# Kernel optimization log

Hardware: AMD Instinct MI355X
Metric: run time of the kernel (lower is better)

The kernel has to match this reference:

```python
import jax, jax.numpy as jnp
import numpy as np

N_FEAT = 350; D = 512; L = 4; DS = 64; NREG = 6; REG_E = 32
B = 32; S = 2048
CLAMP = 20.0


def _ln(x, g, b, eps=1e-5):
    mu = jnp.mean(x, axis=-1, keepdims=True)
    var = jnp.mean(jnp.square(x - mu), axis=-1, keepdims=True)
    return (x - mu) * jax.lax.rsqrt(var + eps) * g + b


def _slstm(x, ln_g, ln_b, Wi, bi, Wf, bf, Wz, bz, Wo, bo, Wp, bp):
    # x: [B,S,D] -> out: [B,S,D]
    xn = _ln(x, ln_g, ln_b)
    log_i = jnp.clip(jnp.einsum('bsd,de->bse', xn, Wi) + bi, -CLAMP, CLAMP)
    log_f = jnp.clip(jnp.einsum('bsd,de->bse', xn, Wf) + bf, -CLAMP, CLAMP)
    z = jnp.tanh(jnp.einsum('bsd,de->bse', xn, Wz) + bz)
    o = jax.nn.sigmoid(jnp.einsum('bsd,de->bse', xn, Wo) + bo)

    def step(carry, inp):
        m, c = carry
        li, lf, zt, ot = inp
        m_new = jnp.maximum(m + lf, li)
        i_s = jnp.exp(li - m_new)
        f_s = jnp.exp(m + lf - m_new)
        c_new = f_s * c + i_s * zt
        h = ot * jnp.tanh(c_new)
        return (m_new, c_new), h

    bsz = x.shape[0]
    init = (jnp.zeros((bsz, DS), x.dtype), jnp.zeros((bsz, DS), x.dtype))
    seq = (jnp.swapaxes(log_i, 0, 1), jnp.swapaxes(log_f, 0, 1),
           jnp.swapaxes(z, 0, 1), jnp.swapaxes(o, 0, 1))
    _, hs = jax.lax.scan(step, init, seq)  # hs: [S,B,DS]
    hs = jnp.swapaxes(hs, 0, 1)  # [B,S,DS]
    return jnp.einsum('bse,ed->bsd', hs, Wp) + bp


def setup_inputs() -> dict:
    key = jax.random.key(0)
    ks = iter(jax.random.split(key, 64))
    def p(*shape):
        return jax.random.normal(next(ks), shape, dtype=jnp.float32) * 0.02
    return {
        'x': jax.random.normal(next(ks), (B, S, N_FEAT), dtype=jnp.float32),
        'regime_ids': jax.random.randint(next(ks), (B, S), 0, NREG),
        'emb_regime': p(NREG, REG_E),
        'grn_w1': p(N_FEAT + REG_E, D), 'grn_b1': jnp.zeros((D,), jnp.float32),
        'grn_w2': p(D, N_FEAT), 'grn_b2': jnp.zeros((N_FEAT,), jnp.float32),
        'in_w': p(N_FEAT, D), 'in_b': jnp.zeros((D,), jnp.float32),
        'ln_in_g': jnp.ones((L, D), jnp.float32), 'ln_in_b': jnp.zeros((L, D), jnp.float32),
        'wi': p(L, D, DS), 'bi': jnp.zeros((L, DS), jnp.float32),
        'wf': p(L, D, DS), 'bf': jnp.zeros((L, DS), jnp.float32),
        'wz': p(L, D, DS), 'bz': jnp.zeros((L, DS), jnp.float32),
        'wo': p(L, D, DS), 'bo': jnp.zeros((L, DS), jnp.float32),
        'wp': p(L, DS, D), 'bp': jnp.zeros((L, D), jnp.float32),
        'nm_g': jnp.ones((L, D), jnp.float32), 'nm_b': jnp.zeros((L, D), jnp.float32),
        'hd15_w': p(D, 1), 'hd15_b': jnp.zeros((1,), jnp.float32),
        'hd30_w': p(D, 1), 'hd30_b': jnp.zeros((1,), jnp.float32),
        'hv_w': p(D, 3), 'hv_b': jnp.zeros((3,), jnp.float32),
        'hreg_w': p(D, NREG), 'hreg_b': jnp.zeros((NREG,), jnp.float32),
        'hrng_w': p(D, 3), 'hrng_b': jnp.zeros((3,), jnp.float32),
    }


def reference(x, regime_ids, emb_regime, grn_w1, grn_b1, grn_w2, grn_b2,
              in_w, in_b, ln_in_g, ln_in_b, wi, bi, wf, bf, wz, bz, wo, bo,
              wp, bp, nm_g, nm_b, hd15_w, hd15_b, hd30_w, hd30_b,
              hv_w, hv_b, hreg_w, hreg_b, hrng_w, hrng_b):
    # Variable selection network (regime-conditioned feature weights)
    remb = emb_regime[regime_ids]                      # [B,S,32]
    comb = jnp.concatenate([x, remb], axis=-1)         # [B,S,382]
    hidden = jax.nn.elu(jnp.einsum('bsf,fd->bsd', comb, grn_w1) + grn_b1)
    weights = jax.nn.softmax(jnp.einsum('bsd,df->bsf', hidden, grn_w2) + grn_b2, axis=-1)
    xw = x * weights
    h = jnp.einsum('bsf,fd->bsd', xw, in_w) + in_b     # [B,S,D]
    for l in range(L):
        res = _slstm(h, ln_in_g[l], ln_in_b[l], wi[l], bi[l], wf[l], bf[l],
                     wz[l], bz[l], wo[l], bo[l], wp[l], bp[l])
        h = _ln(h + res, nm_g[l], nm_b[l])
    h_last = h[:, -1, :]
    return (jnp.squeeze(h_last @ hd15_w + hd15_b, -1),
            jnp.squeeze(h_last @ hd30_w + hd30_b, -1),
            h_last @ hv_w + hv_b,
            h_last @ hreg_w + hreg_b,
            h_last @ hrng_w + hrng_b,
            h_last,
            weights[:, -1, :])
```

## Files before the change

### kernel.cpp

```cpp
#include <hip/hip_runtime.h>
#include <cmath>

#define NFEAT 350
#define DMODEL 512
#define NLAYER 4
#define DSZ 64
#define REG_E 32
#define BATCH 32
#define SEQ 2048
#define MTOK (BATCH * SEQ)
#define CLAMP_V 20.0f

#define CHUNK 64
#define NCHUNK (SEQ / CHUNK)

typedef short bf16x8 __attribute__((ext_vector_type(8)));
typedef float f32x4 __attribute__((ext_vector_type(4)));

__device__ __forceinline__ unsigned short f2b(float v) {
    union { float f; unsigned int u; } x; x.f = v;
    unsigned int r = x.u + 0x7fffu + ((x.u >> 16) & 1u);
    return (unsigned short)(r >> 16);
}
__device__ __forceinline__ float b2f(unsigned short u) {
    union { unsigned int i; float f; } x; x.i = ((unsigned int)u) << 16;
    return x.f;
}
__device__ __forceinline__ unsigned int pack2(float a, float b) {
    return ((unsigned int)f2b(b) << 16) | f2b(a);
}

__global__ __launch_bounds__(256) void tconv_k(const float* __restrict__ src,
                                               unsigned short* __restrict__ dst,
                                               int K, int N, int Kpad) {
    int k = blockIdx.x * 256 + threadIdx.x;
    int n = blockIdx.y;
    if (k >= Kpad) return;
    float v = (k < K && n < N) ? src[(size_t)k * N + n] : 0.f;
    dst[(size_t)n * Kpad + k] = f2b(v);
}

__global__ __launch_bounds__(256) void tconv_g_k(const float* __restrict__ wi,
                                                 const float* __restrict__ wf,
                                                 const float* __restrict__ wz,
                                                 const float* __restrict__ wo,
                                                 unsigned short* __restrict__ dstH,
                                                 unsigned short* __restrict__ dstL) {
    int k = blockIdx.x * 256 + threadIdx.x;
    int n = blockIdx.y;
    int z = blockIdx.z;
    int l = z >> 2, g = z & 3;
    const float* src = (g == 0 ? wi : g == 1 ? wf : g == 2 ? wz : wo) + (size_t)l * DMODEL * DSZ;
    float v = src[(size_t)k * DSZ + n];
    unsigned short hi = f2b(v);
    unsigned short lo = f2b(v - b2f(hi));
    dstH[(size_t)z * 32768 + (size_t)n * 512 + k] = hi;
    dstL[(size_t)z * 32768 + (size_t)n * 512 + k] = lo;
}

__global__ __launch_bounds__(1024) void gbias_k(const float* bi, const float* bf_,
                                                const float* bz, const float* bo,
                                                float* __restrict__ gbias) {
    int t = threadIdx.x;
    int l = t >> 8, r = t & 255, g = r >> 6, e = r & 63;
    const float* s = (g == 0 ? bi : g == 1 ? bf_ : g == 2 ? bz : bo);
    gbias[t] = s[l * 64 + e];
}

__global__ __launch_bounds__(256) void build_xc_k(const float* __restrict__ x,
                                                  const int* __restrict__ rid,
                                                  const float* __restrict__ emb,
                                                  unsigned short* __restrict__ xc) {
    int i = blockIdx.x * 256 + threadIdx.x;
    int m = i / 192, p = i - m * 192;
    int k = p * 2;
    float a = 0.f, b = 0.f;
    if (k < 350) {
        const float2 v = *(const float2*)(x + (size_t)m * NFEAT + k);
        a = v.x; b = v.y;
    } else if (k < 382) {
        int r = rid[m];
        const float2 v = *(const float2*)(emb + r * REG_E + (k - 350));
        a = v.x; b = v.y;
    }
    ((unsigned int*)xc)[(size_t)m * 192 + p] = pack2(a, b);
}

template <int ALD, int EPI>
__global__ __launch_bounds__(256) void mgemm_k(const unsigned short* __restrict__ Ab,
                                               const float* __restrict__ Af,
                                               const unsigned short* __restrict__ Bt,
                                               const float* __restrict__ bias,
                                               float* __restrict__ Cf,
                                               unsigned short* __restrict__ Cb,
                                               const float* __restrict__ muA,
                                               const float* __restrict__ rstdA,
                                               const float* __restrict__ lng,
                                               const float* __restrict__ lnb,
                                               int lda, int ldb, int K, int N, int ldc) {
    __shared__ unsigned short As[128][40];
    __shared__ unsigned short Bs[128][40];
    const int tid = threadIdx.x;
    const int lane = tid & 63;
    const int wave = tid >> 6;
    const int l15 = lane & 15;
    const int quad = lane >> 4;
    const int wm = (wave >> 1) * 64;
    const int wn = (wave & 1) * 64;
    const size_t m0 = (size_t)blockIdx.y * 128;
    const int n0 = blockIdx.x * 128;

    const int sr = tid >> 2;
    const int ku = tid & 3;

    const unsigned short* Br0 = Bt + ((size_t)(n0 + sr)) * ldb + ku * 8;
    const unsigned short* Br1 = Br0 + (size_t)64 * ldb;
    const unsigned short* Ar0 = Ab + (m0 + sr) * (size_t)lda + ku * 8;
    const unsigned short* Ar1 = Ar0 + (size_t)64 * lda;

    f32x4 acc[4][4] = {};

    for (int k0 = 0; k0 < K; k0 += 32) {
        *(uint4*)&As[sr][ku * 8]      = *(const uint4*)(Ar0 + k0);
        *(uint4*)&As[sr + 64][ku * 8] = *(const uint4*)(Ar1 + k0);
        *(uint4*)&Bs[sr][ku * 8]      = *(const uint4*)(Br0 + k0);
        *(uint4*)&Bs[sr + 64][ku * 8] = *(const uint4*)(Br1 + k0);
        __syncthreads();
        bf16x8 af[4], bf[4];
#pragma unroll
        for (int mt = 0; mt < 4; mt++)
            af[mt] = *(const bf16x8*)&As[wm + mt * 16 + l15][quad * 8];
#pragma unroll
        for (int nt = 0; nt < 4; nt++)
            bf[nt] = *(const bf16x8*)&Bs[wn + nt * 16 + l15][quad * 8];
#pragma unroll
        for (int mt = 0; mt < 4; mt++)
#pragma unroll
            for (int nt = 0; nt < 4; nt++)
                acc[mt][nt] = __builtin_amdgcn_mfma_f32_16x16x32_bf16(af[mt], bf[nt], acc[mt][nt], 0, 0, 0);
        __syncthreads();
    }

#pragma unroll
    for (int mt = 0; mt < 4; mt++) {
        int gmb = wm + mt * 16 + quad * 4;
#pragma unroll
        for (int nt = 0; nt < 4; nt++) {
            int gn = n0 + wn + nt * 16 + l15;
            if (gn < N) {
                float bv = bias[gn];
#pragma unroll
                for (int r = 0; r < 4; r++) {
                    size_t gm = m0 + gmb + r;
                    float v = acc[mt][nt][r] + bv;
                    if (EPI == 0) {
                        v = v > 0.f ? v : expm1f(v);
                        Cb[gm * (size_t)ldc + gn] = f2b(v);
                    } else if (EPI == 1) {
                        Cb[gm * (size_t)ldc + gn] = f2b(v);
                    } else {
                        Cf[gm * (size_t)ldc + gn] = v;
                    }
                }
            }
        }
    }
}

__global__ __launch_bounds__(256) void ggemm_k(const float* __restrict__ h,
                                               const unsigned short* __restrict__ BtH,
                                               const unsigned short* __restrict__ BtL,
                                               const float* __restrict__ bias,
                                               const float* __restrict__ mu,
                                               const float* __restrict__ rstd,
                                               const float* __restrict__ lng,
                                               const float* __restrict__ lnb,
                                               float* __restrict__ gates) {
    __shared__ unsigned short AsH[64][40];
    __shared__ unsigned short AsL[64][40];
    __shared__ unsigned short BsH[128][40];
    __shared__ unsigned short BsL[128][40];
    const int tid = threadIdx.x;
    const int lane = tid & 63;
    const int wave = tid >> 6;
    const int l15 = lane & 15;
    const int quad = lane >> 4;
    const int wm = (wave >> 1) * 32;
    const int wn = (wave & 1) * 64;
    const size_t m0 = (size_t)blockIdx.y * 64;
    const int n0 = blockIdx.x * 128;

    const int sr = tid >> 2;
    const int ku = tid & 3;
    const float* Ar = h + (m0 + sr) * (size_t)DMODEL + ku * 8;
    const float muv = mu[m0 + sr];
    const float rsv = rstd[m0 + sr];

    const int br = tid >> 1;
    const int kh = (tid & 1) * 16;
    const unsigned short* BH = BtH + (size_t)(n0 + br) * 512 + kh;
    const unsigned short* BL = BtL + (size_t)(n0 + br) * 512 + kh;

    float4 a0 = *(const float4*)(Ar);
    float4 a1 = *(const float4*)(Ar + 4);
    uint4 vh0 = *(const uint4*)(BH);
    uint4 vh1 = *(const uint4*)(BH + 8);
    uint4 vl0 = *(const uint4*)(BL);
    uint4 vl1 = *(const uint4*)(BL + 8);

    f32x4 acc[2][4] = {};

    for (int k0 = 0; k0 < DMODEL; k0 += 32) {
        {
            float4 g0 = *(const float4*)(lng + k0 + ku * 8);
            float4 g1 = *(const float4*)(lng + k0 + ku * 8 + 4);
            float4 c0 = *(const float4*)(lnb + k0 + ku * 8);
            float4 c1 = *(const float4*)(lnb + k0 + ku * 8 + 4);
            float v[8];
            v[0] = (a0.x - muv) * rsv * g0.x + c0.x;
            v[1] = (a0.y - muv) * rsv * g0.y + c0.y;
            v[2] = (a0.z - muv) * rsv * g0.z + c0.z;
            v[3] = (a0.w - muv) * rsv * g0.w + c0.w;
            v[4] = (a1.x - muv) * rsv * g1.x + c1.x;
            v[5] = (a1.y - muv) * rsv * g1.y + c1.y;
            v[6] = (a1.z - muv) * rsv * g1.z + c1.z;
            v[7] = (a1.w - muv) * rsv * g1.w + c1.w;
            unsigned int hw[4], lw[4];
#pragma unroll
            for (int j = 0; j < 4; j++) {
                unsigned short h0 = f2b(v[2 * j]);
                unsigned short h1 = f2b(v[2 * j + 1]);
                unsigned short l0 = f2b(v[2 * j] - b2f(h0));
                unsigned short l1 = f2b(v[2 * j + 1] - b2f(h1));
                hw[j] = (unsigned int)h0 | ((unsigned int)h1 << 16);
                lw[j] = (unsigned int)l0 | ((unsigned int)l1 << 16);
            }
            *(uint4*)&AsH[sr][ku * 8] = *(uint4*)hw;
            *(uint4*)&AsL[sr][ku * 8] = *(uint4*)lw;
        }
        *(uint4*)&BsH[br][kh]     = vh0;
        *(uint4*)&BsH[br][kh + 8] = vh1;
        *(uint4*)&BsL[br][kh]     = vl0;
        *(uint4*)&BsL[br][kh + 8] = vl1;
        __syncthreads();

        if (k0 + 32 < DMODEL) {
            a0 = *(const float4*)(Ar + k0 + 32);
            a1 = *(const float4*)(Ar + k0 + 36);
            vh0 = *(const uint4*)(BH + k0 + 32);
            vh1 = *(const uint4*)(BH + k0 + 40);
            vl0 = *(const uint4*)(BL + k0 + 32);
            vl1 = *(const uint4*)(BL + k0 + 40);
        }

        bf16x8 ah[2], al[2], bh[4], bl[4];
#pragma unroll
        for (int mt = 0; mt < 2; mt++) {
            ah[mt] = *(const bf16x8*)&AsH[wm + mt * 16 + l15][quad * 8];
            al[mt] = *(const bf16x8*)&AsL[wm + mt * 16 + l15][quad * 8];
        }
#pragma unroll
        for (int nt = 0; nt < 4; nt++) {
            bh[nt] = *(const bf16x8*)&BsH[wn + nt * 16 + l15][quad * 8];
            bl[nt] = *(const bf16x8*)&BsL[wn + nt * 16 + l15][quad * 8];
        }
#pragma unroll
        for (int mt = 0; mt < 2; mt++)
#pragma unroll
            for (int nt = 0; nt < 4; nt++) {
                acc[mt][nt] = __builtin_amdgcn_mfma_f32_16x16x32_bf16(ah[mt], bh[nt], acc[mt][nt], 0, 0, 0);
                acc[mt][nt] = __builtin_amdgcn_mfma_f32_16x16x32_bf16(al[mt], bh[nt], acc[mt][nt], 0, 0, 0);
                acc[mt][nt] = __builtin_amdgcn_mfma_f32_16x16x32_bf16(ah[mt], bl[nt], acc[mt][nt], 0, 0, 0);
            }
        __syncthreads();
    }

#pragma unroll
    for (int mt = 0; mt < 2; mt++) {
        int gmb = wm + mt * 16 + quad * 4;
#pragma unroll
        for (int nt = 0; nt < 4; nt++) {
            int gn = n0 + wn + nt * 16 + l15;
            float bv = bias[gn];
            int g = gn >> 6;
#pragma unroll
            for (int r = 0; r < 4; r++) {
                size_t gm = m0 + gmb + r;
                float v = acc[mt][nt][r] + bv;
                if (g < 2) v = fminf(fmaxf(v, -CLAMP_V), CLAMP_V);
                else if (g == 2) v = tanhf(v);
                else v = 1.f / (1.f + expf(-v));
                gates[gm * 256 + gn] = v;
            }
        }
    }
}

__global__ __launch_bounds__(256) void softmax_xw_k(const unsigned short* __restrict__ logits,
                                                    unsigned short* __restrict__ xc,
                                                    float* __restrict__ out_wlast) {
    int tok = blockIdx.x * 4 + (threadIdx.x >> 6);
    int lane = threadIdx.x & 63;
    const unsigned short* lr = logits + (size_t)tok * NFEAT;
    unsigned short* xr = xc + (size_t)tok * 384;
    float v[6];
    float mx = -1e30f;
#pragma unroll
    for (int i = 0; i < 6; i++) {
        int idx = lane + 64 * i;
        v[i] = (idx < NFEAT) ? b2f(lr[idx]) : -1e30f;
        mx = fmaxf(mx, v[i]);
    }
#pragma unroll
    for (int o = 32; o > 0; o >>= 1) mx = fmaxf(mx, __shfl_xor(mx, o, 64));
    float s = 0.f;
#pragma unroll
    for (int i = 0; i < 6; i++) { v[i] = expf(v[i] - mx); s += v[i]; }
#pragma unroll
    for (int o = 32; o > 0; o >>= 1) s += __shfl_xor(s, o, 64);
    float inv = 1.f / s;
    bool last = ((tok & (SEQ - 1)) == SEQ - 1);
    int b = tok >> 11;
#pragma unroll
    for (int i = 0; i < 6; i++) {
        int idx = lane + 64 * i;
        if (idx < NFEAT) {
            float w = v[i] * inv;
            xr[idx] = f2b(w * b2f(xr[idx]));
            if (last) out_wlast[b * NFEAT + idx] = w;
        } else if (idx < 352) {
            xr[idx] = 0;
        }
    }
}

__global__ __launch_bounds__(256) void ln_stats_k(const float* __restrict__ h,
                                                  float* __restrict__ mu,
                                                  float* __restrict__ rstd) {
    int tok = blockIdx.x * 4 + (threadIdx.x >> 6);
    int lane = threadIdx.x & 63;
    const float* row = h + (size_t)tok * DMODEL;
    float s = 0.f, sq = 0.f;
#pragma unroll
    for (int i = 0; i < 8; i++) {
        float v = row[lane + 64 * i];
        s += v;
        sq += v * v;
    }
#pragma unroll
    for (int o = 32; o > 0; o >>= 1) {
        s += __shfl_xor(s, o, 64);
        sq += __shfl_xor(sq, o, 64);
    }
    if (lane == 0) {
        float m = s * (1.f / DMODEL);
        float var = sq * (1.f / DMODEL) - m * m;
        mu[tok] = m;
        rstd[tok] = rsqrtf(var + 1e-5f);
    }
}

__global__ __launch_bounds__(256) void seg_agg_k(const float* __restrict__ gates,
                                                 float* __restrict__ aggF,
                                                 float* __restrict__ aggL,
                                                 float* __restrict__ aggS) {
    int b = blockIdx.x >> 3;
    int cg = blockIdx.x & 7;
    int chunk = cg * 4 + (threadIdx.x >> 6);
    int e = threadIdx.x & 63;
    const float* gp = gates + ((size_t)b * SEQ + (size_t)chunk * CHUNK) * 256;
    float F = 0.f, L = -1e30f, s = 0.f;
#pragma unroll 4
    for (int t = 0; t < CHUNK; t++) {
        const float* q = gp + (size_t)t * 256;
        float li = q[e], lf = q[64 + e], z = q[128 + e];
        float Ln = fmaxf(L + lf, li);
        s = expf(L + lf - Ln) * s + expf(li - Ln) * z;
        L = Ln;
        F += lf;
    }
    int idx = (b * NCHUNK + chunk) * 64 + e;
    aggF[idx] = F; aggL[idx] = L; aggS[idx] = s;
}

__global__ __launch_bounds__(64) void chunk_scan_k(const float* __restrict__ aggF,
                                                   const float* __restrict__ aggL,
                                                   const float* __restrict__ aggS,
                                                   float* __restrict__ stM,
                                                   float* __restrict__ stC) {
    int b = blockIdx.x;
    int e = threadIdx.x;
    float m = 0.f, c = 0.f;
    for (int k = 0; k < NCHUNK; k++) {
        int idx = (b * NCHUNK + k) * 64 + e;
        stM[idx] = m; stC[idx] = c;
        float F = aggF[idx], L = aggL[idx], s = aggS[idx];
        float mn = fmaxf(m + F, L);
        c = expf(m + F - mn) * c + expf(L - mn) * s;
        m = mn;
    }
}

__global__ __launch_bounds__(256) void replay_k(const float* __restrict__ gates,
                                                const float* __restrict__ stM,
                                                const float* __restrict__ stC,
                                                float* __restrict__ hs) {
    int b = blockIdx.x >> 3;
    int cg = blockIdx.x & 7;
    int chunk = cg * 4 + (threadIdx.x >> 6);
    int e = threadIdx.x & 63;
    int s0 = chunk * CHUNK;
    const float* gp = gates + ((size_t)b * SEQ + s0) * 256;
    float* hp = hs + ((size_t)b * SEQ + s0) * DSZ;
    int idx = (b * NCHUNK + chunk) * 64 + e;
    float m = stM[idx], c = stC[idx];
#pragma unroll 4
    for (int t = 0; t < CHUNK; t++) {
        const float* q = gp + (size_t)t * 256;
        float li = q[e], lf = q[64 + e], z = q[128 + e], o = q[192 + e];
        float mlf = m + lf;
        float mn = fmaxf(mlf, li);
        c = expf(mlf - mn) * c + expf(li - mn) * z;
        m = mn;
        hp[(size_t)t * DSZ + e] = o * tanhf(c);
    }
}

__global__ __launch_bounds__(256) void outproj_k(const float* __restrict__ hs,
                                                 const float* __restrict__ wp,
                                                 const float* __restrict__ bp,
                                                 const float* __restrict__ nmg,
                                                 const float* __restrict__ nmb,
                                                 float* __restrict__ h,
                                                 float* __restrict__ mu,
                                                 float* __restrict__ rstd) {
    __shared__ float shs[16][DSZ];
    __shared__ float swp[16][DMODEL];
    int wv = threadIdx.x >> 6;
    int lane = threadIdx.x & 63;
    int tok0 = blockIdx.x * 16;

    {
        const float4* src = (const float4*)(hs + (size_t)tok0 * DSZ);
        ((float4*)&shs[0][0])[threadIdx.x] = src[threadIdx.x];
    }
    __syncthreads();

    float acc[4][8] = {};
    for (int k0 = 0; k0 < DSZ; k0 += 16) {
        const float4* src = (const float4*)(wp + (size_t)k0 * DMODEL);
#pragma unroll
        for (int i = 0; i < 8; i++)
            ((float4*)&swp[0][0])[threadIdx.x + i * 256] = src[threadIdx.x + i * 256];
        __syncthreads();
#pragma unroll
        for (int k = 0; k < 16; k++) {
            float bv[8];
#pragma unroll
            for (int j = 0; j < 8; j++) bv[j] = swp[k][lane + 64 * j];
#pragma unroll
            for (int t = 0; t < 4; t++) {
                float av = shs[wv * 4 + t][k0 + k];
#pragma unroll
                for (int j = 0; j < 8; j++) acc[t][j] += av * bv[j];
            }
        }
        __syncthreads();
    }

#pragma unroll
    for (int t = 0; t < 4; t++) {
        int tok = tok0 + wv * 4 + t;
        float u[8];
        float s = 0.f, sq = 0.f;
#pragma unroll
        for (int j = 0; j < 8; j++) {
            int col = lane + 64 * j;
            float v = h[(size_t)tok * DMODEL + col] + acc[t][j] + bp[col];
            u[j] = v;
            s += v; sq += v * v;
        }
#pragma unroll
        for (int o = 32; o > 0; o >>= 1) { s += __shfl_xor(s, o, 64); sq += __shfl_xor(sq, o, 64); }
        float mean = s * (1.f / DMODEL);
        float var = sq * (1.f / DMODEL) - mean * mean;
        float rs = rsqrtf(var + 1e-5f);
        float s2 = 0.f, sq2 = 0.f;
#pragma unroll
        for (int j = 0; j < 8; j++) {
            int col = lane + 64 * j;
            float v = (u[j] - mean) * rs * nmg[col] + nmb[col];
            h[(size_t)tok * DMODEL + col] = v;
            s2 += v; sq2 += v * v;
        }
#pragma unroll
        for (int o = 32; o > 0; o >>= 1) { s2 += __shfl_xor(s2, o, 64); sq2 += __shfl_xor(sq2, o, 64); }
        if (lane == 0) {
            float m2 = s2 * (1.f / DMODEL);
            float v2 = sq2 * (1.f / DMODEL) - m2 * m2;
            mu[tok] = m2;
            rstd[tok] = rsqrtf(v2 + 1e-5f);
        }
    }
}

__global__ __launch_bounds__(64) void heads_k(const float* __restrict__ h,
                                              const float* hd15_w, const float* hd15_b,
                                              const float* hd30_w, const float* hd30_b,
                                              const float* hv_w, const float* hv_b,
                                              const float* hreg_w, const float* hreg_b,
                                              const float* hrng_w, const float* hrng_b,
                                              float* __restrict__ out) {
    int b = blockIdx.x;
    int lane = threadIdx.x;
    __shared__ float row[DMODEL];
    const float* hp = h + (size_t)(b * SEQ + SEQ - 1) * DMODEL;
#pragma unroll
    for (int i = 0; i < 8; i++) row[lane + 64 * i] = hp[lane + 64 * i];
    __syncthreads();
#pragma unroll
    for (int i = 0; i < 8; i++) out[448 + b * DMODEL + lane + 64 * i] = row[lane + 64 * i];
    if (lane < 14) {
        const float* w; const float* bb;
        int ncol, j, off;
        if (lane == 0)      { w = hd15_w; bb = hd15_b; ncol = 1; j = 0;         off = 0 + b; }
        else if (lane == 1) { w = hd30_w; bb = hd30_b; ncol = 1; j = 0;         off = 32 + b; }
        else if (lane < 5)  { j = lane - 2;  w = hv_w;   bb = hv_b;   ncol = 3; off = 64 + b * 3 + j; }
        else if (lane < 11) { j = lane - 5;  w = hreg_w; bb = hreg_b; ncol = 6; off = 160 + b * 6 + j; }
        else                { j = lane - 11; w = hrng_w; bb = hrng_b; ncol = 3; off = 352 + b * 3 + j; }
        float s = bb[j];
        for (int k = 0; k < DMODEL; k++) s += row[k] * w[k * ncol + j];
        out[off] = s;
    }
}

extern "C" void kernel_launch(void* const* d_in, const int* in_sizes, int n_in,
                              void* d_out, int out_size, void* d_ws, size_t ws_size,
                              hipStream_t stream) {
    (void)in_sizes; (void)n_in; (void)out_size; (void)ws_size;
    const float* x      = (const float*)d_in[0];
    const int*   rid    = (const int*)d_in[1];
    const float* emb    = (const float*)d_in[2];
    const float* grn_w1 = (const float*)d_in[3];
    const float* grn_b1 = (const float*)d_in[4];
    const float* grn_w2 = (const float*)d_in[5];
    const float* grn_b2 = (const float*)d_in[6];
    const float* in_w   = (const float*)d_in[7];
    const float* in_b   = (const float*)d_in[8];
    const float* ln_g   = (const float*)d_in[9];
    const float* ln_b   = (const float*)d_in[10];
    const float* wi     = (const float*)d_in[11];
    const float* bi     = (const float*)d_in[12];
    const float* wf     = (const float*)d_in[13];
    const float* bf_    = (const float*)d_in[14];
    const float* wz     = (const float*)d_in[15];
    const float* bz     = (const float*)d_in[16];
    const float* wo     = (const float*)d_in[17];
    const float* bo     = (const float*)d_in[18];
    const float* wp     = (const float*)d_in[19];
    const float* bp     = (const float*)d_in[20];
    const float* nm_g   = (const float*)d_in[21];
    const float* nm_b   = (const float*)d_in[22];

    float* out = (float*)d_out;
    char* W = (char*)d_ws;

    float* h               = (float*)W;
    unsigned short* hidden = (unsigned short*)W;
    unsigned short* logits = (unsigned short*)(W + 67108864);
    char* RB = W + 134217728;
    unsigned short* xc = (unsigned short*)RB;
    float* gates  = (float*)RB;
    float* hsbuf  = (float*)(RB + 67108864);
    char* RM = W + 218103808;
    float* aggF  = (float*)(RM);
    float* aggL  = (float*)(RM + 262144);
    float* aggS  = (float*)(RM + 524288);
    float* stM   = (float*)(RM + 786432);
    float* stC   = (float*)(RM + 1048576);
    float* mu    = (float*)(RM + 1310720);
    float* rstd  = (float*)(RM + 1572864);
    unsigned short* w1t  = (unsigned short*)(RM + 1835008);
    unsigned short* w2t  = (unsigned short*)(RM + 2228224);
    unsigned short* inwt = (unsigned short*)(RM + 2621440);
    unsigned short* gwtH = (unsigned short*)(RM + 2981888);
    unsigned short* gwtL = (unsigned short*)(RM + 4030464);
    float* gbias         = (float*)(RM + 5079040);

    build_xc_k<<<MTOK * 192 / 256, 256, 0, stream>>>(x, rid, emb, xc);
    tconv_k<<<dim3(2, 512), 256, 0, stream>>>(grn_w1, w1t, 382, 512, 384);
    tconv_k<<<dim3(2, 384), 256, 0, stream>>>(grn_w2, w2t, 512, 350, 512);
    tconv_k<<<dim3(2, 512), 256, 0, stream>>>(in_w, inwt, 350, 512, 352);
    tconv_g_k<<<dim3(2, 64, 16), 256, 0, stream>>>(wi, wf, wz, wo, gwtH, gwtL);
    gbias_k<<<1, 1024, 0, stream>>>(bi, bf_, bz, bo, gbias);

    mgemm_k<0, 0><<<dim3(4, 512), 256, 0, stream>>>(xc, nullptr, w1t, grn_b1, nullptr, hidden,
                                                    nullptr, nullptr, nullptr, nullptr,
                                                    384, 384, 384, 512, 512);
    mgemm_k<0, 1><<<dim3(3, 512), 256, 0, stream>>>(hidden, nullptr, w2t, grn_b2, nullptr, logits,
                                                    nullptr, nullptr, nullptr, nullptr,
                                                    512, 512, 512, 350, 350);
    softmax_xw_k<<<MTOK / 4, 256, 0, stream>>>(logits, xc, out + 16832);
    mgemm_k<0, 3><<<dim3(4, 512), 256, 0, stream>>>(xc, nullptr, inwt, in_b, h, nullptr,
                                                    nullptr, nullptr, nullptr, nullptr,
                                                    384, 352, 352, 512, 512);
    ln_stats_k<<<MTOK / 4, 256, 0, stream>>>(h, mu, rstd);

    for (int l = 0; l < NLAYER; l++) {
        ggemm_k<<<dim3(2, 1024), 256, 0, stream>>>(h,
                                                   gwtH + (size_t)l * 131072,
                                                   gwtL + (size_t)l * 131072,
                                                   gbias + l * 256,
                                                   mu, rstd,
                                                   ln_g + l * DMODEL, ln_b + l * DMODEL,
                                                   gates);
        seg_agg_k<<<BATCH * 8, 256, 0, stream>>>(gates, aggF, aggL, aggS);
        chunk_scan_k<<<BATCH, 64, 0, stream>>>(aggF, aggL, aggS, stM, stC);
        replay_k<<<BATCH * 8, 256, 0, stream>>>(gates, stM, stC, hsbuf);

        outproj_k<<<MTOK / 16, 256, 0, stream>>>(hsbuf,
                                                 wp + (size_t)l * DSZ * DMODEL,
                                                 bp + l * DMODEL,
                                                 nm_g + l * DMODEL,
                                                 nm_b + l * DMODEL,
                                                 h, mu, rstd);
    }

    heads_k<<<BATCH, 64, 0, stream>>>(h,
                                      (const float*)d_in[23], (const float*)d_in[24],
                                      (const float*)d_in[25], (const float*)d_in[26],
                                      (const float*)d_in[27], (const float*)d_in[28],
                                      (const float*)d_in[29], (const float*)d_in[30],
                                      (const float*)d_in[31], (const float*)d_in[32],
                                      out);
}
```

Measured before the change: 1.483 ms.

## Fuse chunk aggregation into gate GEMM with full-width N tiles

The gate GEMM now computes all 256 gate columns per 64-token block, so each block owns one full chunk. The per-chunk scan aggregate (F, L, s) is then computed in the epilogue from a shared-memory copy of the gates, and the separate seg_agg kernel, which re-read the gates from global memory, is removed. The cost is that each block now loads the whole weight tile, carries larger accumulators and uses about 52KB of shared memory. That lowers occupancy and halves the grid size. The unused mgemm_k template parameter and its arguments are also dropped.

Result: slower. 1.900 ms (+28.1%).

```diff
diff --git a/kernel.cpp b/kernel.cpp
--- a/kernel.cpp
+++ b/kernel.cpp
@@ -86,17 +86,12 @@
     ((unsigned int*)xc)[(size_t)m * 192 + p] = pack2(a, b);
 }
 
-template <int ALD, int EPI>
+template <int EPI>
 __global__ __launch_bounds__(256) void mgemm_k(const unsigned short* __restrict__ Ab,
-                                               const float* __restrict__ Af,
                                                const unsigned short* __restrict__ Bt,
                                                const float* __restrict__ bias,
                                                float* __restrict__ Cf,
                                                unsigned short* __restrict__ Cb,
-                                               const float* __restrict__ muA,
-                                               const float* __restrict__ rstdA,
-                                               const float* __restrict__ lng,
-                                               const float* __restrict__ lnb,
                                                int lda, int ldb, int K, int N, int ldc) {
     __shared__ unsigned short As[128][40];
     __shared__ unsigned short Bs[128][40];
@@ -175,20 +170,24 @@
                                                const float* __restrict__ rstd,
                                                const float* __restrict__ lng,
                                                const float* __restrict__ lnb,
-                                               float* __restrict__ gates) {
-    __shared__ unsigned short AsH[64][40];
-    __shared__ unsigned short AsL[64][40];
-    __shared__ unsigned short BsH[128][40];
-    __shared__ unsigned short BsL[128][40];
+                                               float* __restrict__ gates,
+                                               float* __restrict__ aggF,
+                                               float* __restrict__ aggL,
+                                               float* __restrict__ aggS) {
+    __shared__ __align__(16) char smem[53248];
+    unsigned short* AsH = (unsigned short*)smem;
+    unsigned short* AsL = AsH + 2560;
+    unsigned short* BsH = (unsigned short*)(smem + 10240);
+    unsigned short* BsL = BsH + 10240;
+    float* CP = (float*)smem;
+    float* SG = (float*)(smem + 49152);
+
     const int tid = threadIdx.x;
     const int lane = tid & 63;
     const int wave = tid >> 6;
     const int l15 = lane & 15;
     const int quad = lane >> 4;
-    const int wm = (wave >> 1) * 32;
-    const int wn = (wave & 1) * 64;
-    const size_t m0 = (size_t)blockIdx.y * 64;
-    const int n0 = blockIdx.x * 128;
+    const size_t m0 = (size_t)blockIdx.x * 64;
 
     const int sr = tid >> 2;
     const int ku = tid & 3;
@@ -196,19 +195,19 @@
     const float muv = mu[m0 + sr];
     const float rsv = rstd[m0 + sr];
 
-    const int br = tid >> 1;
-    const int kh = (tid & 1) * 16;
-    const unsigned short* BH = BtH + (size_t)(n0 + br) * 512 + kh;
-    const unsigned short* BL = BtL + (size_t)(n0 + br) * 512 + kh;
+    const unsigned short* BH = BtH + (size_t)tid * 512;
+    const unsigned short* BL = BtL + (size_t)tid * 512;
 
     float4 a0 = *(const float4*)(Ar);
     float4 a1 = *(const float4*)(Ar + 4);
-    uint4 vh0 = *(const uint4*)(BH);
-    uint4 vh1 = *(const uint4*)(BH + 8);
-    uint4 vl0 = *(const uint4*)(BL);
-    uint4 vl1 = *(const uint4*)(BL + 8);
-
-    f32x4 acc[2][4] = {};
+    uint4 vh[4], vl[4];
+#pragma unroll
+    for (int j = 0; j < 4; j++) {
+        vh[j] = *(const uint4*)(BH + j * 8);
+        vl[j] = *(const uint4*)(BL + j * 8);
+    }
+
+    f32x4 acc[4][4] = {};
 
     for (int k0 = 0; k0 < DMODEL; k0 += 32) {
         {
@@ -235,37 +234,40 @@
                 hw[j] = (unsigned int)h0 | ((unsigned int)h1 << 16);
                 lw[j] = (unsigned int)l0 | ((unsigned int)l1 << 16);
             }
-            *(uint4*)&AsH[sr][ku * 8] = *(uint4*)hw;
-            *(uint4*)&AsL[sr][ku * 8] = *(uint4*)lw;
-        }
-        *(uint4*)&BsH[br][kh]     = vh0;
-        *(uint4*)&BsH[br][kh + 8] = vh1;
-        *(uint4*)&BsL[br][kh]     = vl0;
-        *(uint4*)&BsL[br][kh + 8] = vl1;
+            *(uint4*)&AsH[sr * 40 + ku * 8] = *(uint4*)hw;
+            *(uint4*)&AsL[sr * 40 + ku * 8] = *(uint4*)lw;
+        }
+#pragma unroll
+        for (int j = 0; j < 4; j++) {
+            *(uint4*)&BsH[tid * 40 + j * 8] = vh[j];
+            *(uint4*)&BsL[tid * 40 + j * 8] = vl[j];
+        }
         __syncthreads();
 
         if (k0 + 32 < DMODEL) {
             a0 = *(const float4*)(Ar + k0 + 32);
             a1 = *(const float4*)(Ar + k0 + 36);
-            vh0 = *(const uint4*)(BH + k0 + 32);
-            vh1 = *(const uint4*)(BH + k0 + 40);
-            vl0 = *(const uint4*)(BL + k0 + 32);
-            vl1 = *(const uint4*)(BL + k0 + 40);
-        }
-
-        bf16x8 ah[2], al[2], bh[4], bl[4];
-#pragma unroll
-        for (int mt = 0; mt < 2; mt++) {
-            ah[mt] = *(const bf16x8*)&AsH[wm + mt * 16 + l15][quad * 8];
-            al[mt] = *(const bf16x8*)&AsL[wm + mt * 16 + l15][quad * 8];
+#pragma unroll
+            for (int j = 0; j < 4; j++) {
+                vh[j] = *(const uint4*)(BH + k0 + 32 + j * 8);
+                vl[j] = *(const uint4*)(BL + k0 + 32 + j * 8);
+            }
+        }
+
+        bf16x8 ah[4], al[4], bh[4], bl[4];
+#pragma unroll
+        for (int mt = 0; mt < 4; mt++) {
+            ah[mt] = *(const bf16x8*)&AsH[(mt * 16 + l15) * 40 + quad * 8];
+            al[mt] = *(const bf16x8*)&AsL[(mt * 16 + l15) * 40 + quad * 8];
         }
 #pragma unroll
         for (int nt = 0; nt < 4; nt++) {
-            bh[nt] = *(const bf16x8*)&BsH[wn + nt * 16 + l15][quad * 8];
-            bl[nt] = *(const bf16x8*)&BsL[wn + nt * 16 + l15][quad * 8];
-        }
-#pragma unroll
-        for (int mt = 0; mt < 2; mt++)
+            int brow = wave * 64 + nt * 16 + l15;
+            bh[nt] = *(const bf16x8*)&BsH[brow * 40 + quad * 8];
+            bl[nt] = *(const bf16x8*)&BsL[brow * 40 + quad * 8];
+        }
+#pragma unroll
+        for (int mt = 0; mt < 4; mt++)
 #pragma unroll
             for (int nt = 0; nt < 4; nt++) {
                 acc[mt][nt] = __builtin_amdgcn_mfma_f32_16x16x32_bf16(ah[mt], bh[nt], acc[mt][nt], 0, 0, 0);
@@ -276,23 +278,60 @@
     }
 
 #pragma unroll
-    for (int mt = 0; mt < 2; mt++) {
-        int gmb = wm + mt * 16 + quad * 4;
+    for (int mt = 0; mt < 4; mt++) {
 #pragma unroll
         for (int nt = 0; nt < 4; nt++) {
-            int gn = n0 + wn + nt * 16 + l15;
-            float bv = bias[gn];
-            int g = gn >> 6;
+            int e = nt * 16 + l15;
+            int col = wave * 64 + e;
+            float bv = bias[col];
 #pragma unroll
             for (int r = 0; r < 4; r++) {
-                size_t gm = m0 + gmb + r;
+                int row = mt * 16 + quad * 4 + r;
                 float v = acc[mt][nt][r] + bv;
-                if (g < 2) v = fminf(fmaxf(v, -CLAMP_V), CLAMP_V);
-                else if (g == 2) v = tanhf(v);
+                if (wave < 2) v = fminf(fmaxf(v, -CLAMP_V), CLAMP_V);
+                else if (wave == 2) v = tanhf(v);
                 else v = 1.f / (1.f + expf(-v));
-                gates[gm * 256 + gn] = v;
+                gates[(m0 + row) * 256 + col] = v;
+                if (wave < 3) CP[wave * 4096 + row * 64 + e] = v;
             }
         }
+    }
+    __syncthreads();
+
+    {
+        int e = tid & 63;
+        int seg = tid >> 6;
+        float F = 0.f, L = -1e30f, s = 0.f;
+#pragma unroll 4
+        for (int j = 0; j < 16; j++) {
+            int tt = seg * 16 + j;
+            float li = CP[tt * 64 + e];
+            float lf = CP[4096 + tt * 64 + e];
+            float z  = CP[8192 + tt * 64 + e];
+            float Ln = fmaxf(L + lf, li);
+            s = expf(L + lf - Ln) * s + expf(li - Ln) * z;
+            L = Ln;
+            F += lf;
+        }
+        SG[seg * 64 + e]       = F;
+        SG[256 + seg * 64 + e] = L;
+        SG[512 + seg * 64 + e] = s;
+    }
+    __syncthreads();
+    if (tid < 64) {
+        float F = 0.f, L = -1e30f, s = 0.f;
+#pragma unroll
+        for (int k = 0; k < 4; k++) {
+            float Fk = SG[k * 64 + tid];
+            float Lk = SG[256 + k * 64 + tid];
+            float sk = SG[512 + k * 64 + tid];
+            float Ln = fmaxf(L + Fk, Lk);
+            s = expf(L + Fk - Ln) * s + expf(Lk - Ln) * sk;
+            L = Ln;
+            F += Fk;
+        }
+        int idx = blockIdx.x * 64 + tid;
+        aggF[idx] = F; aggL[idx] = L; aggS[idx] = s;
     }
 }
 
@@ -358,29 +397,6 @@
         mu[tok] = m;
         rstd[tok] = rsqrtf(var + 1e-5f);
     }
-}
-
-__global__ __launch_bounds__(256) void seg_agg_k(const float* __restrict__ gates,
-                                                 float* __restrict__ aggF,
-                                                 float* __restrict__ aggL,
-                                                 float* __restrict__ aggS) {
-    int b = blockIdx.x >> 3;
-    int cg = blockIdx.x & 7;
-    int chunk = cg * 4 + (threadIdx.x >> 6);
-    int e = threadIdx.x & 63;
-    const float* gp = gates + ((size_t)b * SEQ + (size_t)chunk * CHUNK) * 256;
-    float F = 0.f, L = -1e30f, s = 0.f;
-#pragma unroll 4
-    for (int t = 0; t < CHUNK; t++) {
-        const float* q = gp + (size_t)t * 256;
-        float li = q[e], lf = q[64 + e], z = q[128 + e];
-        float Ln = fmaxf(L + lf, li);
-        s = expf(L + lf - Ln) * s + expf(li - Ln) * z;
-        L = Ln;
-        F += lf;
-    }
-    int idx = (b * NCHUNK + chunk) * 64 + e;
-    aggF[idx] = F; aggL[idx] = L; aggS[idx] = s;
 }
 
 __global__ __launch_bounds__(64) void chunk_scan_k(const float* __restrict__ aggF,
@@ -594,27 +610,23 @@
     tconv_g_k<<<dim3(2, 64, 16), 256, 0, stream>>>(wi, wf, wz, wo, gwtH, gwtL);
     gbias_k<<<1, 1024, 0, stream>>>(bi, bf_, bz, bo, gbias);
 
-    mgemm_k<0, 0><<<dim3(4, 512), 256, 0, stream>>>(xc, nullptr, w1t, grn_b1, nullptr, hidden,
-                                                    nullptr, nullptr, nullptr, nullptr,
-                                                    384, 384, 384, 512, 512);
-    mgemm_k<0, 1><<<dim3(3, 512), 256, 0, stream>>>(hidden, nullptr, w2t, grn_b2, nullptr, logits,
-                                                    nullptr, nullptr, nullptr, nullptr,
-                                                    512, 512, 512, 350, 350);
+    mgemm_k<0><<<dim3(4, 512), 256, 0, stream>>>(xc, w1t, grn_b1, nullptr, hidden,
+                                                 384, 384, 384, 512, 512);
+    mgemm_k<1><<<dim3(3, 512), 256, 0, stream>>>(hidden, w2t, grn_b2, nullptr, logits,
+                                                 512, 512, 512, 350, 350);
     softmax_xw_k<<<MTOK / 4, 256, 0, stream>>>(logits, xc, out + 16832);
-    mgemm_k<0, 3><<<dim3(4, 512), 256, 0, stream>>>(xc, nullptr, inwt, in_b, h, nullptr,
-                                                    nullptr, nullptr, nullptr, nullptr,
-                                                    384, 352, 352, 512, 512);
+    mgemm_k<3><<<dim3(4, 512), 256, 0, stream>>>(xc, inwt, in_b, h, nullptr,
+                                                 384, 352, 352, 512, 512);
     ln_stats_k<<<MTOK / 4, 256, 0, stream>>>(h, mu, rstd);
 
     for (int l = 0; l < NLAYER; l++) {
-        ggemm_k<<<dim3(2, 1024), 256, 0, stream>>>(h,
-                                                   gwtH + (size_t)l * 131072,
-                                                   gwtL + (size_t)l * 131072,
-                                                   gbias + l * 256,
-                                                   mu, rstd,
-                                                   ln_g + l * DMODEL, ln_b + l * DMODEL,
-                                                   gates);
-        seg_agg_k<<<BATCH * 8, 256, 0, stream>>>(gates, aggF, aggL, aggS);
+        ggemm_k<<<1024, 256, 0, stream>>>(h,
+                                          gwtH + (size_t)l * 131072,
+                                          gwtL + (size_t)l * 131072,
+                                          gbias + l * 256,
+                                          mu, rstd,
+                                          ln_g + l * DMODEL, ln_b + l * DMODEL,
+                                          gates, aggF, aggL, aggS);
         chunk_scan_k<<<BATCH, 64, 0, stream>>>(aggF, aggL, aggS, stM, stC);
         replay_k<<<BATCH * 8, 256, 0, stream>>>(gates, stM, stC, hsbuf);
 
```
